# Kernel optimization log

Hardware: AMD Instinct MI355X
Metric: run time of the kernel (lower is better)

## Reference

```python
import jax, jax.numpy as jnp
import numpy as np

DT_SCALER = 1.0 / 24.0
ODE_STEPS = 4  # fixed-step RK4 stand-in for adaptive odeint(rtol=atol=1e-3)
B, T, D, H = 1024, 100, 32, 256
ODE_MID = 50  # hidden width of the ODE func MLP (hard-coded 50 in source)


def setup_inputs() -> dict:
    key = jax.random.key(0)
    ks = jax.random.split(key, 20)
    n = lambda k, s: jax.random.normal(k, s, dtype=jnp.float32)
    std = 0.1  # module inits weights N(0, 0.1), biases 0
    return {
        "dt": jax.random.uniform(ks[0], (B, T, 2), dtype=jnp.float32),
        "x": n(ks[1], (B, T, D)),
        # RNNCell params
        "W_ih": n(ks[2], (H, D)) * std,
        "b_ih": jnp.zeros((H,), jnp.float32),
        "W_hh": n(ks[3], (H, H)) * std,
        "b_hh": jnp.zeros((H,), jnp.float32),
        # ODE func: Linear(H,50) -> tanh -> Linear(50,H)
        "ode_w1": n(ks[4], (ODE_MID, H)) * std,
        "ode_b1": jnp.zeros((ODE_MID,), jnp.float32),
        "ode_w2": n(ks[5], (H, ODE_MID)) * std,
        "ode_b2": jnp.zeros((H,), jnp.float32),
        # mu head: l1 (H -> H//2), distribution_mu (H//2 -> 1)
        "l1_w": n(ks[6], (H // 2, H)) * std,
        "l1_b": jnp.zeros((H // 2,), jnp.float32),
        "mu_w": n(ks[7], (1, H // 2)) * std,
        "mu_b": jnp.zeros((1,), jnp.float32),
        # sigma head: Linear(H,H) -> tanh -> Linear(H,1) -> softplus
        "sig_w1": n(ks[8], (H, H)) * std,
        "sig_b1": jnp.zeros((H,), jnp.float32),
        "sig_w2": n(ks[9], (1, H)) * std,
        "sig_b2": jnp.zeros((1,), jnp.float32),
    }


def reference(dt, x, W_ih, b_ih, W_hh, b_hh, ode_w1, ode_b1, ode_w2, ode_b2,
              l1_w, l1_b, mu_w, mu_b, sig_w1, sig_b1, sig_w2, sig_b2):
    Bsz = x.shape[0]
    xs = jnp.swapaxes(x, 0, 1)                               # [T,B,D]
    dts = jnp.swapaxes(dt[:, :, 1] - dt[:, :, 0], 0, 1)[..., None]  # [T,B,1]
    h0 = jnp.zeros((Bsz, W_hh.shape[0]), x.dtype)
    hs = 1.0 / ODE_STEPS

    def ode_f(y, scale):
        # net(y) * (dt * DT_SCALER); RHS is time-independent
        return (jnp.tanh(y @ ode_w1.T + ode_b1) @ ode_w2.T + ode_b2) * scale

    def step(h, inp):
        x_i, dt_i = inp                                      # [B,D], [B,1]
        # h_t = h_t + RNNCell(x_i, h_t)
        h = h + jnp.tanh(x_i @ W_ih.T + b_ih + h @ W_hh.T + b_hh)
        scale = dt_i * DT_SCALER
        # integrate dh/dt = ode_f(h) from t=0 to t=1 (fixed-step RK4)
        def rk4(y, _):
            k1 = ode_f(y, scale)
            k2 = ode_f(y + 0.5 * hs * k1, scale)
            k3 = ode_f(y + 0.5 * hs * k2, scale)
            k4 = ode_f(y + hs * k3, scale)
            return y + (hs / 6.0) * (k1 + 2.0 * k2 + 2.0 * k3 + k4), None
        h, _ = jax.lax.scan(rk4, h, None, length=ODE_STEPS)
        # heads (eval mode: dropout is identity)
        mu = jax.nn.relu(h @ l1_w.T + l1_b) @ mu_w.T + mu_b              # [B,1]
        sig = jax.nn.softplus(jnp.tanh(h @ sig_w1.T + sig_b1) @ sig_w2.T + sig_b2)
        return h, (mu, sig)

    _, (mu_seq, sig_seq) = jax.lax.scan(step, h0, (xs, dts))
    mu_out = jnp.swapaxes(mu_seq, 0, 1)    # [B,T,1]
    sig_out = jnp.swapaxes(sig_seq, 0, 1)  # [B,T,1]
    return (mu_out, sig_out)
```

## Files before the change

### kernel.cpp

```cpp
#include <hip/hip_runtime.h>
#include <math.h>


#define NT 512

#define WS_WCAT 0
#define WS_L1P  73728
#define WS_SW1  106496
#define WS_TOT  172032

#define SM_PR  0
#define SM_H   8192
#define SM_YC  8704
#define SM_AC  9216
#define SM_MD  9728
#define SM_X4  9856
#define SM_BC  9920
#define SM_OB1 10176
#define SM_OB2 10240
#define SM_L1B 10496
#define SM_SB1 10624
#define SM_MUW 10880
#define SM_SW2 11008
#define SM_SCL 11264
#define SM_TOT 11272
#define SMEM_BYTES (SM_TOT * 4)

__device__ __forceinline__ float fma4(float acc, float4 y, float4 w) {
  acc = fmaf(y.x, w.x, acc);
  acc = fmaf(y.y, w.y, acc);
  acc = fmaf(y.z, w.z, acc);
  acc = fmaf(y.w, w.w, acc);
  return acc;
}

__device__ __forceinline__ float4 add4(float4 a, float4 b) {
  return make_float4(a.x + b.x, a.y + b.y, a.z + b.z, a.w + b.w);
}

__device__ __forceinline__ float tfast(float x) {
  float ax = fabsf(x);
  float e  = __expf(-2.f * ax);
  float t  = (1.f - e) * __builtin_amdgcn_rcpf(1.f + e);
  return copysignf(t, x);
}

__device__ __forceinline__ float4 tfast4(float4 v) {
  return make_float4(tfast(v.x), tfast(v.y), tfast(v.z), tfast(v.w));
}

__global__ void prep_transpose(const float* __restrict__ Wih,
                               const float* __restrict__ Whh,
                               const float* __restrict__ l1w,
                               const float* __restrict__ sw1,
                               float* __restrict__ ws) {
  int i = blockIdx.x * 256 + threadIdx.x;
  if (i < 73728) {
    int g = i >> 10, rem = i & 1023, j = rem >> 2, c = rem & 3;
    int k = 4 * g + c;
    ws[i] = (k < 32) ? Wih[j * 32 + k] : Whh[j * 256 + (k - 32)];
  } else if (i < 106496) {
    int t = i - 73728;
    int g = t >> 9, rem = t & 511, j = rem >> 2, c = rem & 3;
    ws[i] = l1w[j * 256 + 4 * g + c];
  } else if (i < WS_TOT) {
    int t = i - 106496;
    int g = t >> 10, rem = t & 1023, j = rem >> 2, c = rem & 3;
    ws[i] = sw1[j * 256 + 4 * g + c];
  }
}

__global__ __attribute__((amdgpu_flat_work_group_size(NT, NT)))
__attribute__((amdgpu_waves_per_eu(4)))
void odernn_main(const float* __restrict__ dt,
                 const float* __restrict__ x,
                 const float* __restrict__ bih,
                 const float* __restrict__ bhh,
                 const float* __restrict__ ow1,
                 const float* __restrict__ ob1g,
                 const float* __restrict__ ow2,
                 const float* __restrict__ ob2g,
                 const float* __restrict__ l1bg,
                 const float* __restrict__ muwg,
                 const float* __restrict__ mubg,
                 const float* __restrict__ sb1g,
                 const float* __restrict__ sw2g,
                 const float* __restrict__ sb2g,
                 const float* __restrict__ ws,
                 float* __restrict__ out) {
  extern __shared__ __align__(16) float sm[];
  const int tid = threadIdx.x;
  const int wv = tid >> 6, ln = tid & 63;
  const int b0 = blockIdx.x * 2;

  float* hS   = sm + SM_H;
  float* x4S  = sm + SM_X4;
  float* bcS  = sm + SM_BC;
  float* ob1S = sm + SM_OB1;
  float* ob2S = sm + SM_OB2;
  float* l1bS = sm + SM_L1B;
  float* sb1S = sm + SM_SB1;
  float* muwS = sm + SM_MUW;
  float* sw2S = sm + SM_SW2;
  float* sclS = sm + SM_SCL;

  float4* pr4  = (float4*)(sm + SM_PR);
  float4* h4   = (float4*)(sm + SM_H);
  float4* yc4  = (float4*)(sm + SM_YC);
  float4* ac4  = (float4*)(sm + SM_AC);
  float4* md4w = (float4*)(sm + SM_MD);
  float4* l1o4 = (float4*)(sm + SM_YC);
  float4* sg4  = (float4*)(sm + SM_AC);
  const float4* h44  = (const float4*)(sm + SM_H);
  const float4* yc44 = (const float4*)(sm + SM_YC);
  const float4* md4  = (const float4*)(sm + SM_MD);
  const float4* x44  = (const float4*)(sm + SM_X4);
  const float4* bc4  = (const float4*)bcS;
  const float4* ob1_4 = (const float4*)ob1S;
  const float4* ob2_4 = (const float4*)ob2S;
  const float4* l1b4 = (const float4*)l1bS;
  const float4* sb14 = (const float4*)sb1S;
  const float4* muw4 = (const float4*)muwS;
  const float4* sw24 = (const float4*)sw2S;

  const float4* wcat4 = (const float4*)(ws + WS_WCAT);
  const float4* l1w4  = (const float4*)(ws + WS_L1P);
  const float4* sw14  = (const float4*)(ws + WS_SW1);

  const int q1 = tid & 15, kc1 = tid >> 4;
  const int cq2 = tid & 63, kc2 = tid >> 6;
  float4 w1r[4][2];
  float4 w2r[4][2];
  {
#pragma unroll
    for (int n = 0; n < 4; ++n) {
      int row = 4 * q1 + n;
#pragma unroll
      for (int g = 0; g < 2; ++g) {
        if (row < 50)
          w1r[n][g] = *(const float4*)&ow1[row * 256 + kc1 * 8 + 4 * g];
        else
          w1r[n][g] = make_float4(0.f, 0.f, 0.f, 0.f);
      }
    }
    float w2tmp[4];
#pragma unroll
    for (int n = 0; n < 4; ++n) {
      int col = 4 * cq2 + n;
#pragma unroll
      for (int g = 0; g < 2; ++g) {
#pragma unroll
        for (int c = 0; c < 4; ++c) {
          int k = kc2 * 8 + 4 * g + c;
          w2tmp[c] = (k < 50) ? ow2[col * 50 + k] : 0.f;
        }
        w2r[n][g] = make_float4(w2tmp[0], w2tmp[1], w2tmp[2], w2tmp[3]);
      }
    }
  }

  if (tid < 256) {
    bcS[tid]  = bih[tid] + bhh[tid];
    ob2S[tid] = ob2g[tid];
    sb1S[tid] = sb1g[tid];
    sw2S[tid] = sw2g[tid];
  }
  if (tid < 64)  ob1S[tid] = (tid < 50) ? ob1g[tid] : 0.f;
  if (tid < 128) { l1bS[tid] = l1bg[tid]; muwS[tid] = muwg[tid]; }
  if (tid < 512) hS[tid] = 0.f;
  __syncthreads();

  const float mub = mubg[0], sb2 = sb2g[0];

  for (int t = 0; t < 100; ++t) {
    if (tid < 64) {
      int r = tid >> 5, kk = tid & 31;
      x4S[r * 32 + kk] = x[((size_t)(b0 + r) * 100 + t) * 32 + kk];
    }
    if (tid < 2) {
      const float* dp = dt + ((size_t)(b0 + tid) * 100 + t) * 2;
      sclS[tid] = (dp[1] - dp[0]) * (1.f / 24.f);
    }
    __syncthreads();

    {
      const int jq = tid & 63, kc = tid >> 6;
      float4 acc0 = make_float4(0, 0, 0, 0), acc1 = acc0;
#pragma unroll 3
      for (int gg = 0; gg < 9; ++gg) {
        int g = kc * 9 + gg;
        float4 w0 = wcat4[g * 256 + 4 * jq + 0];
        float4 w1 = wcat4[g * 256 + 4 * jq + 1];
        float4 w2 = wcat4[g * 256 + 4 * jq + 2];
        float4 w3 = wcat4[g * 256 + 4 * jq + 3];
        float4 y0 = (g < 8) ? x44[g]     : h44[g - 8];
        float4 y1 = (g < 8) ? x44[8 + g] : h44[64 + (g - 8)];
        acc0.x = fma4(acc0.x, y0, w0); acc0.y = fma4(acc0.y, y0, w1);
        acc0.z = fma4(acc0.z, y0, w2); acc0.w = fma4(acc0.w, y0, w3);
        acc1.x = fma4(acc1.x, y1, w0); acc1.y = fma4(acc1.y, y1, w1);
        acc1.z = fma4(acc1.z, y1, w2); acc1.w = fma4(acc1.w, y1, w3);
      }
      pr4[(kc * 2 + 0) * 64 + jq] = acc0;
      pr4[(kc * 2 + 1) * 64 + jq] = acc1;
    }
    __syncthreads();
    if (tid < 128) {
      const int r = tid >> 6, jq = tid & 63;
      float4 v = pr4[r * 64 + jq];
#pragma unroll
      for (int kc = 1; kc < 8; ++kc) v = add4(v, pr4[(kc * 2 + r) * 64 + jq]);
      v = add4(v, bc4[jq]);
      int o4 = r * 64 + jq;
      h4[o4] = add4(h4[o4], tfast4(v));
    }
    __syncthreads();

#pragma unroll 1
    for (int os = 0; os < 4; ++os) {
#pragma unroll
      for (int s = 0; s < 4; ++s) {
        {
          const float4* ysrc = (s == 0) ? h44 : yc44;
          float4 a0 = make_float4(0, 0, 0, 0), a1 = a0;
#pragma unroll
          for (int g = 0; g < 2; ++g) {
            float4 y0 = ysrc[kc1 * 2 + g];
            float4 y1 = ysrc[64 + kc1 * 2 + g];
            a0.x = fma4(a0.x, y0, w1r[0][g]); a0.y = fma4(a0.y, y0, w1r[1][g]);
            a0.z = fma4(a0.z, y0, w1r[2][g]); a0.w = fma4(a0.w, y0, w1r[3][g]);
            a1.x = fma4(a1.x, y1, w1r[0][g]); a1.y = fma4(a1.y, y1, w1r[1][g]);
            a1.z = fma4(a1.z, y1, w1r[2][g]); a1.w = fma4(a1.w, y1, w1r[3][g]);
          }
          pr4[(kc1 * 2 + 0) * 16 + q1] = a0;
          pr4[(kc1 * 2 + 1) * 16 + q1] = a1;
        }
        __syncthreads();
        if (tid < 128) {
          const int r = tid >> 6, sub = (tid >> 4) & 3, qq = tid & 15;
          float4 v = pr4[(sub * 8 * 2 + r) * 16 + qq];
#pragma unroll
          for (int i = 1; i < 8; ++i)
            v = add4(v, pr4[((sub * 8 + i) * 2 + r) * 16 + qq]);
          v.x += __shfl_xor(v.x, 16); v.y += __shfl_xor(v.y, 16);
          v.z += __shfl_xor(v.z, 16); v.w += __shfl_xor(v.w, 16);
          v.x += __shfl_xor(v.x, 32); v.y += __shfl_xor(v.y, 32);
          v.z += __shfl_xor(v.z, 32); v.w += __shfl_xor(v.w, 32);
          if (sub == 0)
            md4w[r * 16 + qq] = tfast4(add4(v, ob1_4[qq]));
        }
        __syncthreads();
        {
          float4 b0v = make_float4(0, 0, 0, 0), b1v = b0v;
#pragma unroll
          for (int g = 0; g < 2; ++g) {
            float4 m0 = md4[kc2 * 2 + g];
            float4 m1 = md4[16 + kc2 * 2 + g];
            b0v.x = fma4(b0v.x, m0, w2r[0][g]); b0v.y = fma4(b0v.y, m0, w2r[1][g]);
            b0v.z = fma4(b0v.z, m0, w2r[2][g]); b0v.w = fma4(b0v.w, m0, w2r[3][g]);
            b1v.x = fma4(b1v.x, m1, w2r[0][g]); b1v.y = fma4(b1v.y, m1, w2r[1][g]);
            b1v.z = fma4(b1v.z, m1, w2r[2][g]); b1v.w = fma4(b1v.w, m1, w2r[3][g]);
          }
          pr4[(kc2 * 2 + 0) * 64 + cq2] = b0v;
          pr4[(kc2 * 2 + 1) * 64 + cq2] = b1v;
        }
        __syncthreads();
        if (tid < 128) {
          const int r = tid >> 6, cq = tid & 63;
          float4 v = pr4[r * 64 + cq];
#pragma unroll
          for (int kc = 1; kc < 8; ++kc) v = add4(v, pr4[(kc * 2 + r) * 64 + cq]);
          v = add4(v, ob2_4[cq]);
          float sc = sclS[r];
          float4 kv = make_float4(v.x * sc, v.y * sc, v.z * sc, v.w * sc);
          int o4 = r * 64 + cq;
          if (s == 0) {
            ac4[o4] = kv;
            float4 hv = h4[o4];
            yc4[o4] = make_float4(hv.x + 0.125f * kv.x, hv.y + 0.125f * kv.y,
                                  hv.z + 0.125f * kv.z, hv.w + 0.125f * kv.w);
          } else if (s == 1) {
            float4 a = ac4[o4];
            ac4[o4] = make_float4(a.x + 2.f * kv.x, a.y + 2.f * kv.y,
                                  a.z + 2.f * kv.z, a.w + 2.f * kv.w);
            float4 hv = h4[o4];
            yc4[o4] = make_float4(hv.x + 0.125f * kv.x, hv.y + 0.125f * kv.y,
                                  hv.z + 0.125f * kv.z, hv.w + 0.125f * kv.w);
          } else if (s == 2) {
            float4 a = ac4[o4];
            ac4[o4] = make_float4(a.x + 2.f * kv.x, a.y + 2.f * kv.y,
                                  a.z + 2.f * kv.z, a.w + 2.f * kv.w);
            float4 hv = h4[o4];
            yc4[o4] = make_float4(hv.x + 0.25f * kv.x, hv.y + 0.25f * kv.y,
                                  hv.z + 0.25f * kv.z, hv.w + 0.25f * kv.w);
          } else {
            float4 a = ac4[o4];
            float4 hv = h4[o4];
            const float c6 = 0.25f / 6.f;
            h4[o4] = make_float4(hv.x + c6 * (a.x + kv.x), hv.y + c6 * (a.y + kv.y),
                                 hv.z + c6 * (a.z + kv.z), hv.w + c6 * (a.w + kv.w));
          }
        }
        __syncthreads();
      }
    }

    {
      const int cq = tid & 31, kc = tid >> 5;
      float4 c0 = make_float4(0, 0, 0, 0), c1 = c0;
#pragma unroll 2
      for (int g = 0; g < 4; ++g) {
        int kg = kc * 4 + g;
        float4 w0 = l1w4[kg * 128 + 4 * cq + 0];
        float4 w1 = l1w4[kg * 128 + 4 * cq + 1];
        float4 w2 = l1w4[kg * 128 + 4 * cq + 2];
        float4 w3 = l1w4[kg * 128 + 4 * cq + 3];
        float4 y0 = h44[kg], y1 = h44[64 + kg];
        c0.x = fma4(c0.x, y0, w0); c0.y = fma4(c0.y, y0, w1);
        c0.z = fma4(c0.z, y0, w2); c0.w = fma4(c0.w, y0, w3);
        c1.x = fma4(c1.x, y1, w0); c1.y = fma4(c1.y, y1, w1);
        c1.z = fma4(c1.z, y1, w2); c1.w = fma4(c1.w, y1, w3);
      }
      pr4[(kc * 2 + 0) * 32 + cq] = c0;
      pr4[(kc * 2 + 1) * 32 + cq] = c1;
    }
    {
      float4 d0 = make_float4(0, 0, 0, 0), d1 = d0;
#pragma unroll 2
      for (int g = 0; g < 8; ++g) {
        int kg = kc2 * 8 + g;
        float4 w0 = sw14[kg * 256 + 4 * cq2 + 0];
        float4 w1 = sw14[kg * 256 + 4 * cq2 + 1];
        float4 w2 = sw14[kg * 256 + 4 * cq2 + 2];
        float4 w3 = sw14[kg * 256 + 4 * cq2 + 3];
        float4 y0 = h44[kg], y1 = h44[64 + kg];
        d0.x = fma4(d0.x, y0, w0); d0.y = fma4(d0.y, y0, w1);
        d0.z = fma4(d0.z, y0, w2); d0.w = fma4(d0.w, y0, w3);
        d1.x = fma4(d1.x, y1, w0); d1.y = fma4(d1.y, y1, w1);
        d1.z = fma4(d1.z, y1, w2); d1.w = fma4(d1.w, y1, w3);
      }
      pr4[1024 + (kc2 * 2 + 0) * 64 + cq2] = d0;
      pr4[1024 + (kc2 * 2 + 1) * 64 + cq2] = d1;
    }
    __syncthreads();
    if (tid < 128) {
      const int r = tid >> 6, sub = (tid >> 5) & 1, cq = tid & 31;
      float4 v = pr4[(sub * 8 * 2 + r) * 32 + cq];
#pragma unroll
      for (int i = 1; i < 8; ++i)
        v = add4(v, pr4[((sub * 8 + i) * 2 + r) * 32 + cq]);
      v.x += __shfl_xor(v.x, 32); v.y += __shfl_xor(v.y, 32);
      v.z += __shfl_xor(v.z, 32); v.w += __shfl_xor(v.w, 32);
      if (sub == 0) {
        float4 b = l1b4[cq];
        l1o4[r * 32 + cq] = make_float4(fmaxf(v.x + b.x, 0.f), fmaxf(v.y + b.y, 0.f),
                                        fmaxf(v.z + b.z, 0.f), fmaxf(v.w + b.w, 0.f));
      }
    } else if (tid < 256) {
      const int t2 = tid - 128;
      const int r = t2 >> 6, cq = t2 & 63;
      float4 v = pr4[1024 + r * 64 + cq];
#pragma unroll
      for (int kc = 1; kc < 8; ++kc)
        v = add4(v, pr4[1024 + (kc * 2 + r) * 64 + cq]);
      sg4[r * 64 + cq] = tfast4(add4(v, sb14[cq]));
    }
    __syncthreads();
    if (wv < 2) {
      const int r = wv, c = ln & 31;
      float4 l = l1o4[r * 32 + c], w = muw4[c];
      float pm = (ln < 32) ? (l.x * w.x + l.y * w.y + l.z * w.z + l.w * w.w) : 0.f;
#pragma unroll
      for (int off = 32; off > 0; off >>= 1) pm += __shfl_down(pm, off);
      if (ln == 0) out[(size_t)(b0 + r) * 100 + t] = pm + mub;
    } else if (wv < 4) {
      const int r = wv - 2;
      float4 s4 = sg4[r * 64 + ln], w = sw24[ln];
      float ps = s4.x * w.x + s4.y * w.y + s4.z * w.z + s4.w * w.w;
#pragma unroll
      for (int off = 32; off > 0; off >>= 1) ps += __shfl_down(ps, off);
      if (ln == 0) {
        float z = ps + sb2;
        float sp = fmaxf(z, 0.f) + log1pf(expf(-fabsf(z)));
        out[(size_t)102400 + (size_t)(b0 + r) * 100 + t] = sp;
      }
    }
  }
}

extern "C" void kernel_launch(void* const* d_in, const int* in_sizes, int n_in,
                              void* d_out, int out_size, void* d_ws, size_t ws_size,
                              hipStream_t stream) {
  const float* dt  = (const float*)d_in[0];
  const float* x   = (const float*)d_in[1];
  const float* Wih = (const float*)d_in[2];
  const float* bih = (const float*)d_in[3];
  const float* Whh = (const float*)d_in[4];
  const float* bhh = (const float*)d_in[5];
  const float* ow1 = (const float*)d_in[6];
  const float* ob1 = (const float*)d_in[7];
  const float* ow2 = (const float*)d_in[8];
  const float* ob2 = (const float*)d_in[9];
  const float* l1w = (const float*)d_in[10];
  const float* l1b = (const float*)d_in[11];
  const float* muw = (const float*)d_in[12];
  const float* mub = (const float*)d_in[13];
  const float* sw1 = (const float*)d_in[14];
  const float* sb1 = (const float*)d_in[15];
  const float* sw2 = (const float*)d_in[16];
  const float* sb2 = (const float*)d_in[17];
  float* ws  = (float*)d_ws;
  float* out = (float*)d_out;

  hipFuncSetAttribute((const void*)odernn_main,
                      hipFuncAttributeMaxDynamicSharedMemorySize, SMEM_BYTES);

  prep_transpose<<<WS_TOT / 256, 256, 0, stream>>>(Wih, Whh, l1w, sw1, ws);
  odernn_main<<<512, NT, SMEM_BYTES, stream>>>(dt, x, bih, bhh, ow1, ob1, ow2, ob2,
                                               l1b, muw, mub, sb1, sw2, sb2, ws, out);
}
```

Baseline: 3.755 ms.

## Split ODE MLP layers across half-block producer/consumer groups with DPP reductions

Rewrites the main kernel so the first 256 threads compute the ODE first layer and the mu head, while the other 256 compute the second layer, RK4 update and sigma head. Each half is synchronised through a single shared buffer. Cross-lane partial-sum reductions now use DPP adds instead of shared-memory partial buffers plus extra reduce passes. The RNN weights are re-laid out so each thread reads a contiguous float4 stream. H is double-buffered, and x/dt for the next step are prefetched, with the aim of cutting the shared-memory footprint and barrier count. The divergent split relies on matched __syncthreads counts between the two groups, which is fragile.

```diff
diff --git a/kernel.cpp b/kernel.cpp
--- a/kernel.cpp
+++ b/kernel.cpp
@@ -4,69 +4,124 @@
 
 #define NT 512
 
-#define WS_WCAT 0
-#define WS_L1P  73728
-#define WS_SW1  106496
-#define WS_TOT  172032
-
-#define SM_PR  0
-#define SM_H   8192
-#define SM_YC  8704
-#define SM_AC  9216
-#define SM_MD  9728
-#define SM_X4  9856
-#define SM_BC  9920
-#define SM_OB1 10176
-#define SM_OB2 10240
-#define SM_L1B 10496
-#define SM_SB1 10624
-#define SM_MUW 10880
-#define SM_SW2 11008
-#define SM_SCL 11264
-#define SM_TOT 11272
-#define SMEM_BYTES (SM_TOT * 4)
+#define WF_WCAT 0
+#define WF_L1   18432
+#define WF_SG   26624
+
+#define F4_YC   0
+#define F4_MID  128
+#define F4_HL   160
+#define F4_X    416
+#define F4_L1O  432
+#define F4_SG   496
+#define SM_L1B  2496
+#define SM_SB1  2624
+#define SM_MUW  2880
+#define SM_SW2  3008
+#define SM_SCL  3264
+#define SM_TOTF 3272
 
 __device__ __forceinline__ float fma4(float acc, float4 y, float4 w) {
-  acc = fmaf(y.x, w.x, acc);
-  acc = fmaf(y.y, w.y, acc);
-  acc = fmaf(y.z, w.z, acc);
-  acc = fmaf(y.w, w.w, acc);
+  acc = fmaf(y.x, w.x, acc); acc = fmaf(y.y, w.y, acc);
+  acc = fmaf(y.z, w.z, acc); acc = fmaf(y.w, w.w, acc);
   return acc;
 }
-
 __device__ __forceinline__ float4 add4(float4 a, float4 b) {
   return make_float4(a.x + b.x, a.y + b.y, a.z + b.z, a.w + b.w);
 }
-
+__device__ __forceinline__ float4 axpy4(float a, float4 xv, float4 yv) {
+  return make_float4(fmaf(a, xv.x, yv.x), fmaf(a, xv.y, yv.y),
+                     fmaf(a, xv.z, yv.z), fmaf(a, xv.w, yv.w));
+}
+__device__ __forceinline__ float4 muls4(float4 v, float s) {
+  return make_float4(v.x * s, v.y * s, v.z * s, v.w * s);
+}
 __device__ __forceinline__ float tfast(float x) {
   float ax = fabsf(x);
   float e  = __expf(-2.f * ax);
   float t  = (1.f - e) * __builtin_amdgcn_rcpf(1.f + e);
   return copysignf(t, x);
 }
-
 __device__ __forceinline__ float4 tfast4(float4 v) {
   return make_float4(tfast(v.x), tfast(v.y), tfast(v.z), tfast(v.w));
 }
 
-__global__ void prep_transpose(const float* __restrict__ Wih,
-                               const float* __restrict__ Whh,
-                               const float* __restrict__ l1w,
-                               const float* __restrict__ sw1,
-                               float* __restrict__ ws) {
+template <int CTRL>
+__device__ __forceinline__ float dpp_add(float v) {
+  int s = __builtin_amdgcn_update_dpp(0, __float_as_int(v), CTRL, 0xF, 0xF, true);
+  return v + __int_as_float(s);
+}
+__device__ __forceinline__ float red2(float v)  { return dpp_add<0xB1>(v); }
+__device__ __forceinline__ float red4(float v)  { return dpp_add<0x4E>(dpp_add<0xB1>(v)); }
+__device__ __forceinline__ float red8(float v)  {
+  return dpp_add<0xB1>(dpp_add<0x4E>(dpp_add<0x141>(v)));
+}
+__device__ __forceinline__ float red16(float v) {
+  return dpp_add<0xB1>(dpp_add<0x4E>(dpp_add<0x141>(dpp_add<0x140>(v))));
+}
+
+__global__ void prep_w(const float* __restrict__ Wih, const float* __restrict__ Whh,
+                       const float* __restrict__ l1w, const float* __restrict__ sw1,
+                       float* __restrict__ ws) {
   int i = blockIdx.x * 256 + threadIdx.x;
   if (i < 73728) {
-    int g = i >> 10, rem = i & 1023, j = rem >> 2, c = rem & 3;
-    int k = 4 * g + c;
-    ws[i] = (k < 32) ? Wih[j * 32 + k] : Whh[j * 256 + (k - 32)];
-  } else if (i < 106496) {
+    int fi = i >> 2, comp = i & 3;
+    int j = fi >> 9, tw = fi & 511;
+    int c = j / 9, gg = j - c * 9;
+    int cq = tw >> 3, kc = tw & 7;
+    int k = 36 * kc + 4 * gg + comp, col = 4 * cq + c;
+    ws[i] = (k < 32) ? Wih[col * 32 + k] : Whh[col * 256 + (k - 32)];
+  } else if (i < 73728 + 32768) {
     int t = i - 73728;
-    int g = t >> 9, rem = t & 511, j = rem >> 2, c = rem & 3;
-    ws[i] = l1w[j * 256 + 4 * g + c];
-  } else if (i < WS_TOT) {
+    int fi = t >> 2, comp = t & 3;
+    int j = fi >> 7, tt = fi & 127;
+    int c = j >> 4, jj = j & 15;
+    int cq = tt >> 2, kc = tt & 3;
+    int k = 4 * (4 * jj + kc) + comp, col = 4 * cq + c;
+    ws[73728 + t] = l1w[col * 256 + k];
+  } else if (i < 172032) {
     int t = i - 106496;
-    int g = t >> 10, rem = t & 1023, j = rem >> 2, c = rem & 3;
-    ws[i] = sw1[j * 256 + 4 * g + c];
+    int fi = t >> 2, comp = t & 3;
+    int j = fi >> 7, tt = fi & 127;
+    int c = j >> 5, jj = j & 31;
+    int cq = tt >> 1, kc = tt & 1;
+    int k = 4 * (2 * jj + kc) + comp, col = 4 * cq + c;
+    ws[106496 + t] = sw1[col * 256 + k];
+  }
+}
+
+__device__ __forceinline__ void rnn_phase(int tid, int pOld, const float4* __restrict__ wc4,
+                                          float4* smf4, float4 bcR) {
+  const int cq = tid >> 3, kc = tid & 7;
+  float a0 = 0, a1 = 0, a2 = 0, a3 = 0, a4 = 0, a5 = 0, a6 = 0, a7 = 0;
+#pragma unroll 1
+  for (int gg = 0; gg < 9; ++gg) {
+    int g = kc * 9 + gg;
+    int i0 = (g < 8) ? (F4_X + g) : (F4_HL + pOld * 128 + (g - 8));
+    int i1 = (g < 8) ? (F4_X + 8 + g) : (F4_HL + pOld * 128 + 64 + (g - 8));
+    float4 y0 = smf4[i0];
+    float4 y1 = smf4[i1];
+    float4 w0 = wc4[(0 * 9 + gg) * 512 + tid];
+    float4 w1 = wc4[(1 * 9 + gg) * 512 + tid];
+    float4 w2 = wc4[(2 * 9 + gg) * 512 + tid];
+    float4 w3 = wc4[(3 * 9 + gg) * 512 + tid];
+    a0 = fma4(a0, y0, w0); a1 = fma4(a1, y0, w1);
+    a2 = fma4(a2, y0, w2); a3 = fma4(a3, y0, w3);
+    a4 = fma4(a4, y1, w0); a5 = fma4(a5, y1, w1);
+    a6 = fma4(a6, y1, w2); a7 = fma4(a7, y1, w3);
+  }
+  a0 = red8(a0); a1 = red8(a1); a2 = red8(a2); a3 = red8(a3);
+  a4 = red8(a4); a5 = red8(a5); a6 = red8(a6); a7 = red8(a7);
+  if (kc == 0) {
+    float4 h0 = smf4[F4_HL + pOld * 128 + cq];
+    float4 h1 = smf4[F4_HL + pOld * 128 + 64 + cq];
+    float4 n0 = add4(h0, tfast4(add4(make_float4(a0, a1, a2, a3), bcR)));
+    float4 n1 = add4(h1, tfast4(add4(make_float4(a4, a5, a6, a7), bcR)));
+    int pN = pOld ^ 1;
+    smf4[F4_HL + pN * 128 + cq] = n0;
+    smf4[F4_HL + pN * 128 + 64 + cq] = n1;
+    smf4[F4_YC + cq] = n0;
+    smf4[F4_YC + 64 + cq] = n1;
   }
 }
 
@@ -88,300 +143,222 @@
                  const float* __restrict__ sb2g,
                  const float* __restrict__ ws,
                  float* __restrict__ out) {
-  extern __shared__ __align__(16) float sm[];
+  __shared__ __align__(16) float sm[SM_TOTF];
+  float4* smf4 = (float4*)sm;
   const int tid = threadIdx.x;
-  const int wv = tid >> 6, ln = tid & 63;
   const int b0 = blockIdx.x * 2;
 
-  float* hS   = sm + SM_H;
-  float* x4S  = sm + SM_X4;
-  float* bcS  = sm + SM_BC;
-  float* ob1S = sm + SM_OB1;
-  float* ob2S = sm + SM_OB2;
-  float* l1bS = sm + SM_L1B;
-  float* sb1S = sm + SM_SB1;
-  float* muwS = sm + SM_MUW;
-  float* sw2S = sm + SM_SW2;
-  float* sclS = sm + SM_SCL;
-
-  float4* pr4  = (float4*)(sm + SM_PR);
-  float4* h4   = (float4*)(sm + SM_H);
-  float4* yc4  = (float4*)(sm + SM_YC);
-  float4* ac4  = (float4*)(sm + SM_AC);
-  float4* md4w = (float4*)(sm + SM_MD);
-  float4* l1o4 = (float4*)(sm + SM_YC);
-  float4* sg4  = (float4*)(sm + SM_AC);
-  const float4* h44  = (const float4*)(sm + SM_H);
-  const float4* yc44 = (const float4*)(sm + SM_YC);
-  const float4* md4  = (const float4*)(sm + SM_MD);
-  const float4* x44  = (const float4*)(sm + SM_X4);
-  const float4* bc4  = (const float4*)bcS;
-  const float4* ob1_4 = (const float4*)ob1S;
-  const float4* ob2_4 = (const float4*)ob2S;
-  const float4* l1b4 = (const float4*)l1bS;
-  const float4* sb14 = (const float4*)sb1S;
-  const float4* muw4 = (const float4*)muwS;
-  const float4* sw24 = (const float4*)sw2S;
-
-  const float4* wcat4 = (const float4*)(ws + WS_WCAT);
-  const float4* l1w4  = (const float4*)(ws + WS_L1P);
-  const float4* sw14  = (const float4*)(ws + WS_SW1);
-
-  const int q1 = tid & 15, kc1 = tid >> 4;
-  const int cq2 = tid & 63, kc2 = tid >> 6;
-  float4 w1r[4][2];
-  float4 w2r[4][2];
-  {
+  const float4* wc4  = (const float4*)ws + WF_WCAT;
+  const float4* l1s4 = (const float4*)ws + WF_L1;
+  const float4* sgs4 = (const float4*)ws + WF_SG;
+
+  const int cqR = tid >> 3;
+  float4 bcR = make_float4(bih[4 * cqR + 0] + bhh[4 * cqR + 0],
+                           bih[4 * cqR + 1] + bhh[4 * cqR + 1],
+                           bih[4 * cqR + 2] + bhh[4 * cqR + 2],
+                           bih[4 * cqR + 3] + bhh[4 * cqR + 3]);
+
+  if (tid < 128) { sm[SM_L1B + tid] = l1bg[tid]; sm[SM_MUW + tid] = muwg[tid]; }
+  if (tid < 256) { sm[SM_SB1 + tid] = sb1g[tid]; sm[SM_SW2 + tid] = sw2g[tid]; }
+  if (tid < 128) smf4[F4_HL + tid] = make_float4(0.f, 0.f, 0.f, 0.f);
+  if (tid < 16) {
+    int r = tid >> 3, g = tid & 7;
+    smf4[F4_X + tid] = ((const float4*)x)[((size_t)(b0 + r) * 100) * 8 + g];
+  } else if (tid < 18) {
+    const float* dp = dt + ((size_t)(b0 + tid - 16) * 100) * 2;
+    sm[SM_SCL + tid - 16] = (dp[1] - dp[0]) * (1.f / 24.f);
+  }
+  __syncthreads();
+
+  if (tid < 256) {
+    const int q1 = tid >> 4, kc1 = tid & 15;
+    float4 w1r[16];
 #pragma unroll
     for (int n = 0; n < 4; ++n) {
       int row = 4 * q1 + n;
 #pragma unroll
-      for (int g = 0; g < 2; ++g) {
-        if (row < 50)
-          w1r[n][g] = *(const float4*)&ow1[row * 256 + kc1 * 8 + 4 * g];
-        else
-          w1r[n][g] = make_float4(0.f, 0.f, 0.f, 0.f);
-      }
+      for (int j = 0; j < 4; ++j)
+        w1r[n * 4 + j] = (row < 50)
+            ? *(const float4*)&ow1[row * 256 + 64 * j + 4 * kc1]
+            : make_float4(0.f, 0.f, 0.f, 0.f);
     }
-    float w2tmp[4];
-#pragma unroll
-    for (int n = 0; n < 4; ++n) {
-      int col = 4 * cq2 + n;
-#pragma unroll
-      for (int g = 0; g < 2; ++g) {
-#pragma unroll
-        for (int c = 0; c < 4; ++c) {
-          int k = kc2 * 8 + 4 * g + c;
-          w2tmp[c] = (k < 50) ? ow2[col * 50 + k] : 0.f;
-        }
-        w2r[n][g] = make_float4(w2tmp[0], w2tmp[1], w2tmp[2], w2tmp[3]);
+    float4 ob1r = make_float4(4 * q1 + 0 < 50 ? ob1g[4 * q1 + 0] : 0.f,
+                              4 * q1 + 1 < 50 ? ob1g[4 * q1 + 1] : 0.f,
+                              4 * q1 + 2 < 50 ? ob1g[4 * q1 + 2] : 0.f,
+                              4 * q1 + 3 < 50 ? ob1g[4 * q1 + 3] : 0.f);
+    const int rH = tid >> 7, cqH = (tid >> 2) & 31, kcH = tid & 3;
+    const int t7 = tid & 127;
+    const float mubv = mubg[0];
+
+    for (int t = 0; t < 100; ++t) {
+      const int pOld = t & 1, pNew = pOld ^ 1;
+      rnn_phase(tid, pOld, wc4, smf4, bcR);
+      __syncthreads();
+#pragma unroll 1
+      for (int e = 0; e < 16; ++e) {
+        float a0 = 0, a1 = 0, a2 = 0, a3 = 0, a4 = 0, a5 = 0, a6 = 0, a7 = 0;
+#pragma unroll
+        for (int j = 0; j < 4; ++j) {
+          float4 y0 = smf4[F4_YC + 16 * j + kc1];
+          float4 y1 = smf4[F4_YC + 64 + 16 * j + kc1];
+          a0 = fma4(a0, y0, w1r[0 * 4 + j]); a1 = fma4(a1, y0, w1r[1 * 4 + j]);
+          a2 = fma4(a2, y0, w1r[2 * 4 + j]); a3 = fma4(a3, y0, w1r[3 * 4 + j]);
+          a4 = fma4(a4, y1, w1r[0 * 4 + j]); a5 = fma4(a5, y1, w1r[1 * 4 + j]);
+          a6 = fma4(a6, y1, w1r[2 * 4 + j]); a7 = fma4(a7, y1, w1r[3 * 4 + j]);
+        }
+        a0 = red16(a0); a1 = red16(a1); a2 = red16(a2); a3 = red16(a3);
+        a4 = red16(a4); a5 = red16(a5); a6 = red16(a6); a7 = red16(a7);
+        if (kc1 == 0) {
+          smf4[F4_MID + q1]      = tfast4(add4(make_float4(a0, a1, a2, a3), ob1r));
+          smf4[F4_MID + 16 + q1] = tfast4(add4(make_float4(a4, a5, a6, a7), ob1r));
+        }
+        __syncthreads();
+        __syncthreads();
+      }
+      float c0 = 0, c1 = 0, c2 = 0, c3 = 0;
+#pragma unroll 2
+      for (int jj = 0; jj < 16; ++jj) {
+        float4 h = smf4[F4_HL + pNew * 128 + rH * 64 + 4 * jj + kcH];
+        c0 = fma4(c0, h, l1s4[(0 * 16 + jj) * 128 + t7]);
+        c1 = fma4(c1, h, l1s4[(1 * 16 + jj) * 128 + t7]);
+        c2 = fma4(c2, h, l1s4[(2 * 16 + jj) * 128 + t7]);
+        c3 = fma4(c3, h, l1s4[(3 * 16 + jj) * 128 + t7]);
+      }
+      c0 = red4(c0); c1 = red4(c1); c2 = red4(c2); c3 = red4(c3);
+      if (kcH == 0) {
+        float4 b = ((const float4*)(sm + SM_L1B))[cqH];
+        float4 v = add4(make_float4(c0, c1, c2, c3), b);
+        smf4[F4_L1O + rH * 32 + cqH] =
+            make_float4(fmaxf(v.x, 0.f), fmaxf(v.y, 0.f), fmaxf(v.z, 0.f), fmaxf(v.w, 0.f));
+      }
+      if (t < 99) {
+        if (tid < 16) {
+          int r = tid >> 3, g = tid & 7;
+          smf4[F4_X + tid] = ((const float4*)x)[((size_t)(b0 + r) * 100 + t + 1) * 8 + g];
+        } else if (tid < 18) {
+          const float* dp = dt + ((size_t)(b0 + tid - 16) * 100 + t + 1) * 2;
+          sm[SM_SCL + tid - 16] = (dp[1] - dp[0]) * (1.f / 24.f);
+        }
+      }
+      __syncthreads();
+      int wv = tid >> 6, ln = tid & 63;
+      if (wv < 2) {
+        float pm = 0.f;
+        if (ln < 32) {
+          float4 l = smf4[F4_L1O + wv * 32 + ln];
+          float4 w = ((const float4*)(sm + SM_MUW))[ln];
+          pm = l.x * w.x + l.y * w.y + l.z * w.z + l.w * w.w;
+        }
+#pragma unroll
+        for (int off = 32; off > 0; off >>= 1) pm += __shfl_down(pm, off);
+        if (ln == 0) out[(size_t)(b0 + wv) * 100 + t] = pm + mubv;
       }
     }
-  }
-
-  if (tid < 256) {
-    bcS[tid]  = bih[tid] + bhh[tid];
-    ob2S[tid] = ob2g[tid];
-    sb1S[tid] = sb1g[tid];
-    sw2S[tid] = sw2g[tid];
-  }
-  if (tid < 64)  ob1S[tid] = (tid < 50) ? ob1g[tid] : 0.f;
-  if (tid < 128) { l1bS[tid] = l1bg[tid]; muwS[tid] = muwg[tid]; }
-  if (tid < 512) hS[tid] = 0.f;
-  __syncthreads();
-
-  const float mub = mubg[0], sb2 = sb2g[0];
-
-  for (int t = 0; t < 100; ++t) {
-    if (tid < 64) {
-      int r = tid >> 5, kk = tid & 31;
-      x4S[r * 32 + kk] = x[((size_t)(b0 + r) * 100 + t) * 32 + kk];
+  } else {
+    const int tid2 = tid - 256;
+    const int cqB = tid2 >> 2, kc2 = tid2 & 3;
+    float4 w2r[16];
+#pragma unroll
+    for (int c = 0; c < 4; ++c) {
+      int col = 4 * cqB + c;
+#pragma unroll
+      for (int j = 0; j < 4; ++j) {
+        float w0v[4];
+#pragma unroll
+        for (int cc = 0; cc < 4; ++cc) {
+          int k = 16 * j + 4 * kc2 + cc;
+          w0v[cc] = (k < 50) ? ow2[col * 50 + k] : 0.f;
+        }
+        w2r[c * 4 + j] = make_float4(w0v[0], w0v[1], w0v[2], w0v[3]);
+      }
     }
-    if (tid < 2) {
-      const float* dp = dt + ((size_t)(b0 + tid) * 100 + t) * 2;
-      sclS[tid] = (dp[1] - dp[0]) * (1.f / 24.f);
-    }
-    __syncthreads();
-
-    {
-      const int jq = tid & 63, kc = tid >> 6;
-      float4 acc0 = make_float4(0, 0, 0, 0), acc1 = acc0;
-#pragma unroll 3
-      for (int gg = 0; gg < 9; ++gg) {
-        int g = kc * 9 + gg;
-        float4 w0 = wcat4[g * 256 + 4 * jq + 0];
-        float4 w1 = wcat4[g * 256 + 4 * jq + 1];
-        float4 w2 = wcat4[g * 256 + 4 * jq + 2];
-        float4 w3 = wcat4[g * 256 + 4 * jq + 3];
-        float4 y0 = (g < 8) ? x44[g]     : h44[g - 8];
-        float4 y1 = (g < 8) ? x44[8 + g] : h44[64 + (g - 8)];
-        acc0.x = fma4(acc0.x, y0, w0); acc0.y = fma4(acc0.y, y0, w1);
-        acc0.z = fma4(acc0.z, y0, w2); acc0.w = fma4(acc0.w, y0, w3);
-        acc1.x = fma4(acc1.x, y1, w0); acc1.y = fma4(acc1.y, y1, w1);
-        acc1.z = fma4(acc1.z, y1, w2); acc1.w = fma4(acc1.w, y1, w3);
-      }
-      pr4[(kc * 2 + 0) * 64 + jq] = acc0;
-      pr4[(kc * 2 + 1) * 64 + jq] = acc1;
-    }
-    __syncthreads();
-    if (tid < 128) {
-      const int r = tid >> 6, jq = tid & 63;
-      float4 v = pr4[r * 64 + jq];
-#pragma unroll
-      for (int kc = 1; kc < 8; ++kc) v = add4(v, pr4[(kc * 2 + r) * 64 + jq]);
-      v = add4(v, bc4[jq]);
-      int o4 = r * 64 + jq;
-      h4[o4] = add4(h4[o4], tfast4(v));
-    }
-    __syncthreads();
-
+    float4 ob2r = make_float4(ob2g[4 * cqB + 0], ob2g[4 * cqB + 1],
+                              ob2g[4 * cqB + 2], ob2g[4 * cqB + 3]);
+    const int rH = tid2 >> 7, cqH = (tid2 >> 1) & 63, kcH = tid2 & 1;
+    const int t7 = tid2 & 127;
+    const float sb2v = sb2g[0];
+
+    for (int t = 0; t < 100; ++t) {
+      const int pOld = t & 1, pNew = pOld ^ 1;
+      rnn_phase(tid, pOld, wc4, smf4, bcR);
+      __syncthreads();
+      float s0 = sm[SM_SCL + 0], s1 = sm[SM_SCL + 1];
+      float4 h0 = smf4[F4_YC + cqB];
+      float4 h1 = smf4[F4_YC + 64 + cqB];
+      float4 ac0 = make_float4(0, 0, 0, 0), ac1 = ac0;
 #pragma unroll 1
-    for (int os = 0; os < 4; ++os) {
-#pragma unroll
-      for (int s = 0; s < 4; ++s) {
-        {
-          const float4* ysrc = (s == 0) ? h44 : yc44;
-          float4 a0 = make_float4(0, 0, 0, 0), a1 = a0;
-#pragma unroll
-          for (int g = 0; g < 2; ++g) {
-            float4 y0 = ysrc[kc1 * 2 + g];
-            float4 y1 = ysrc[64 + kc1 * 2 + g];
-            a0.x = fma4(a0.x, y0, w1r[0][g]); a0.y = fma4(a0.y, y0, w1r[1][g]);
-            a0.z = fma4(a0.z, y0, w1r[2][g]); a0.w = fma4(a0.w, y0, w1r[3][g]);
-            a1.x = fma4(a1.x, y1, w1r[0][g]); a1.y = fma4(a1.y, y1, w1r[1][g]);
-            a1.z = fma4(a1.z, y1, w1r[2][g]); a1.w = fma4(a1.w, y1, w1r[3][g]);
+      for (int os = 0; os < 4; ++os) {
+#pragma unroll
+        for (int s = 0; s < 4; ++s) {
+          __syncthreads();
+          float b0 = 0, b1 = 0, b2 = 0, b3 = 0, b4 = 0, b5 = 0, b6 = 0, b7 = 0;
+#pragma unroll
+          for (int j = 0; j < 4; ++j) {
+            float4 m0 = smf4[F4_MID + 4 * j + kc2];
+            float4 m1 = smf4[F4_MID + 16 + 4 * j + kc2];
+            b0 = fma4(b0, m0, w2r[0 * 4 + j]); b1 = fma4(b1, m0, w2r[1 * 4 + j]);
+            b2 = fma4(b2, m0, w2r[2 * 4 + j]); b3 = fma4(b3, m0, w2r[3 * 4 + j]);
+            b4 = fma4(b4, m1, w2r[0 * 4 + j]); b5 = fma4(b5, m1, w2r[1 * 4 + j]);
+            b6 = fma4(b6, m1, w2r[2 * 4 + j]); b7 = fma4(b7, m1, w2r[3 * 4 + j]);
           }
-          pr4[(kc1 * 2 + 0) * 16 + q1] = a0;
-          pr4[(kc1 * 2 + 1) * 16 + q1] = a1;
-        }
-        __syncthreads();
-        if (tid < 128) {
-          const int r = tid >> 6, sub = (tid >> 4) & 3, qq = tid & 15;
-          float4 v = pr4[(sub * 8 * 2 + r) * 16 + qq];
-#pragma unroll
-          for (int i = 1; i < 8; ++i)
-            v = add4(v, pr4[((sub * 8 + i) * 2 + r) * 16 + qq]);
-          v.x += __shfl_xor(v.x, 16); v.y += __shfl_xor(v.y, 16);
-          v.z += __shfl_xor(v.z, 16); v.w += __shfl_xor(v.w, 16);
-          v.x += __shfl_xor(v.x, 32); v.y += __shfl_xor(v.y, 32);
-          v.z += __shfl_xor(v.z, 32); v.w += __shfl_xor(v.w, 32);
-          if (sub == 0)
-            md4w[r * 16 + qq] = tfast4(add4(v, ob1_4[qq]));
-        }
-        __syncthreads();
-        {
-          float4 b0v = make_float4(0, 0, 0, 0), b1v = b0v;
-#pragma unroll
-          for (int g = 0; g < 2; ++g) {
-            float4 m0 = md4[kc2 * 2 + g];
-            float4 m1 = md4[16 + kc2 * 2 + g];
-            b0v.x = fma4(b0v.x, m0, w2r[0][g]); b0v.y = fma4(b0v.y, m0, w2r[1][g]);
-            b0v.z = fma4(b0v.z, m0, w2r[2][g]); b0v.w = fma4(b0v.w, m0, w2r[3][g]);
-            b1v.x = fma4(b1v.x, m1, w2r[0][g]); b1v.y = fma4(b1v.y, m1, w2r[1][g]);
-            b1v.z = fma4(b1v.z, m1, w2r[2][g]); b1v.w = fma4(b1v.w, m1, w2r[3][g]);
+          b0 = red4(b0); b1 = red4(b1); b2 = red4(b2); b3 = red4(b3);
+          b4 = red4(b4); b5 = red4(b5); b6 = red4(b6); b7 = red4(b7);
+          float4 k0 = muls4(add4(make_float4(b0, b1, b2, b3), ob2r), s0);
+          float4 k1 = muls4(add4(make_float4(b4, b5, b6, b7), ob2r), s1);
+          float4 y0w, y1w;
+          if (s == 0) {
+            ac0 = k0; ac1 = k1;
+            y0w = axpy4(0.125f, k0, h0); y1w = axpy4(0.125f, k1, h1);
+          } else if (s == 1) {
+            ac0 = axpy4(2.f, k0, ac0); ac1 = axpy4(2.f, k1, ac1);
+            y0w = axpy4(0.125f, k0, h0); y1w = axpy4(0.125f, k1, h1);
+          } else if (s == 2) {
+            ac0 = axpy4(2.f, k0, ac0); ac1 = axpy4(2.f, k1, ac1);
+            y0w = axpy4(0.25f, k0, h0); y1w = axpy4(0.25f, k1, h1);
+          } else {
+            h0 = axpy4(0.25f / 6.f, add4(ac0, k0), h0);
+            h1 = axpy4(0.25f / 6.f, add4(ac1, k1), h1);
+            y0w = h0; y1w = h1;
           }
-          pr4[(kc2 * 2 + 0) * 64 + cq2] = b0v;
-          pr4[(kc2 * 2 + 1) * 64 + cq2] = b1v;
-        }
-        __syncthreads();
-        if (tid < 128) {
-          const int r = tid >> 6, cq = tid & 63;
-          float4 v = pr4[r * 64 + cq];
-#pragma unroll
-          for (int kc = 1; kc < 8; ++kc) v = add4(v, pr4[(kc * 2 + r) * 64 + cq]);
-          v = add4(v, ob2_4[cq]);
-          float sc = sclS[r];
-          float4 kv = make_float4(v.x * sc, v.y * sc, v.z * sc, v.w * sc);
-          int o4 = r * 64 + cq;
-          if (s == 0) {
-            ac4[o4] = kv;
-            float4 hv = h4[o4];
-            yc4[o4] = make_float4(hv.x + 0.125f * kv.x, hv.y + 0.125f * kv.y,
-                                  hv.z + 0.125f * kv.z, hv.w + 0.125f * kv.w);
-          } else if (s == 1) {
-            float4 a = ac4[o4];
-            ac4[o4] = make_float4(a.x + 2.f * kv.x, a.y + 2.f * kv.y,
-                                  a.z + 2.f * kv.z, a.w + 2.f * kv.w);
-            float4 hv = h4[o4];
-            yc4[o4] = make_float4(hv.x + 0.125f * kv.x, hv.y + 0.125f * kv.y,
-                                  hv.z + 0.125f * kv.z, hv.w + 0.125f * kv.w);
-          } else if (s == 2) {
-            float4 a = ac4[o4];
-            ac4[o4] = make_float4(a.x + 2.f * kv.x, a.y + 2.f * kv.y,
-                                  a.z + 2.f * kv.z, a.w + 2.f * kv.w);
-            float4 hv = h4[o4];
-            yc4[o4] = make_float4(hv.x + 0.25f * kv.x, hv.y + 0.25f * kv.y,
-                                  hv.z + 0.25f * kv.z, hv.w + 0.25f * kv.w);
-          } else {
-            float4 a = ac4[o4];
-            float4 hv = h4[o4];
-            const float c6 = 0.25f / 6.f;
-            h4[o4] = make_float4(hv.x + c6 * (a.x + kv.x), hv.y + c6 * (a.y + kv.y),
-                                 hv.z + c6 * (a.z + kv.z), hv.w + c6 * (a.w + kv.w));
+          if (kc2 == 0) {
+            smf4[F4_YC + cqB] = y0w;
+            smf4[F4_YC + 64 + cqB] = y1w;
+            if (os == 3 && s == 3) {
+              smf4[F4_HL + pNew * 128 + cqB] = h0;
+              smf4[F4_HL + pNew * 128 + 64 + cqB] = h1;
+            }
           }
-        }
-        __syncthreads();
-      }
-    }
-
-    {
-      const int cq = tid & 31, kc = tid >> 5;
-      float4 c0 = make_float4(0, 0, 0, 0), c1 = c0;
+          __syncthreads();
+        }
+      }
+      float d0 = 0, d1 = 0, d2 = 0, d3 = 0;
 #pragma unroll 2
-      for (int g = 0; g < 4; ++g) {
-        int kg = kc * 4 + g;
-        float4 w0 = l1w4[kg * 128 + 4 * cq + 0];
-        float4 w1 = l1w4[kg * 128 + 4 * cq + 1];
-        float4 w2 = l1w4[kg * 128 + 4 * cq + 2];
-        float4 w3 = l1w4[kg * 128 + 4 * cq + 3];
-        float4 y0 = h44[kg], y1 = h44[64 + kg];
-        c0.x = fma4(c0.x, y0, w0); c0.y = fma4(c0.y, y0, w1);
-        c0.z = fma4(c0.z, y0, w2); c0.w = fma4(c0.w, y0, w3);
-        c1.x = fma4(c1.x, y1, w0); c1.y = fma4(c1.y, y1, w1);
-        c1.z = fma4(c1.z, y1, w2); c1.w = fma4(c1.w, y1, w3);
-      }
-      pr4[(kc * 2 + 0) * 32 + cq] = c0;
-      pr4[(kc * 2 + 1) * 32 + cq] = c1;
-    }
-    {
-      float4 d0 = make_float4(0, 0, 0, 0), d1 = d0;
-#pragma unroll 2
-      for (int g = 0; g < 8; ++g) {
-        int kg = kc2 * 8 + g;
-        float4 w0 = sw14[kg * 256 + 4 * cq2 + 0];
-        float4 w1 = sw14[kg * 256 + 4 * cq2 + 1];
-        float4 w2 = sw14[kg * 256 + 4 * cq2 + 2];
-        float4 w3 = sw14[kg * 256 + 4 * cq2 + 3];
-        float4 y0 = h44[kg], y1 = h44[64 + kg];
-        d0.x = fma4(d0.x, y0, w0); d0.y = fma4(d0.y, y0, w1);
-        d0.z = fma4(d0.z, y0, w2); d0.w = fma4(d0.w, y0, w3);
-        d1.x = fma4(d1.x, y1, w0); d1.y = fma4(d1.y, y1, w1);
-        d1.z = fma4(d1.z, y1, w2); d1.w = fma4(d1.w, y1, w3);
-      }
-      pr4[1024 + (kc2 * 2 + 0) * 64 + cq2] = d0;
-      pr4[1024 + (kc2 * 2 + 1) * 64 + cq2] = d1;
-    }
-    __syncthreads();
-    if (tid < 128) {
-      const int r = tid >> 6, sub = (tid >> 5) & 1, cq = tid & 31;
-      float4 v = pr4[(sub * 8 * 2 + r) * 32 + cq];
-#pragma unroll
-      for (int i = 1; i < 8; ++i)
-        v = add4(v, pr4[((sub * 8 + i) * 2 + r) * 32 + cq]);
-      v.x += __shfl_xor(v.x, 32); v.y += __shfl_xor(v.y, 32);
-      v.z += __shfl_xor(v.z, 32); v.w += __shfl_xor(v.w, 32);
-      if (sub == 0) {
-        float4 b = l1b4[cq];
-        l1o4[r * 32 + cq] = make_float4(fmaxf(v.x + b.x, 0.f), fmaxf(v.y + b.y, 0.f),
-                                        fmaxf(v.z + b.z, 0.f), fmaxf(v.w + b.w, 0.f));
-      }
-    } else if (tid < 256) {
-      const int t2 = tid - 128;
-      const int r = t2 >> 6, cq = t2 & 63;
-      float4 v = pr4[1024 + r * 64 + cq];
-#pragma unroll
-      for (int kc = 1; kc < 8; ++kc)
-        v = add4(v, pr4[1024 + (kc * 2 + r) * 64 + cq]);
-      sg4[r * 64 + cq] = tfast4(add4(v, sb14[cq]));
-    }
-    __syncthreads();
-    if (wv < 2) {
-      const int r = wv, c = ln & 31;
-      float4 l = l1o4[r * 32 + c], w = muw4[c];
-      float pm = (ln < 32) ? (l.x * w.x + l.y * w.y + l.z * w.z + l.w * w.w) : 0.f;
-#pragma unroll
-      for (int off = 32; off > 0; off >>= 1) pm += __shfl_down(pm, off);
-      if (ln == 0) out[(size_t)(b0 + r) * 100 + t] = pm + mub;
-    } else if (wv < 4) {
-      const int r = wv - 2;
-      float4 s4 = sg4[r * 64 + ln], w = sw24[ln];
-      float ps = s4.x * w.x + s4.y * w.y + s4.z * w.z + s4.w * w.w;
-#pragma unroll
-      for (int off = 32; off > 0; off >>= 1) ps += __shfl_down(ps, off);
-      if (ln == 0) {
-        float z = ps + sb2;
-        float sp = fmaxf(z, 0.f) + log1pf(expf(-fabsf(z)));
-        out[(size_t)102400 + (size_t)(b0 + r) * 100 + t] = sp;
+      for (int jj = 0; jj < 32; ++jj) {
+        float4 h = smf4[F4_HL + pNew * 128 + rH * 64 + 2 * jj + kcH];
+        d0 = fma4(d0, h, sgs4[(0 * 32 + jj) * 128 + t7]);
+        d1 = fma4(d1, h, sgs4[(1 * 32 + jj) * 128 + t7]);
+        d2 = fma4(d2, h, sgs4[(2 * 32 + jj) * 128 + t7]);
+        d3 = fma4(d3, h, sgs4[(3 * 32 + jj) * 128 + t7]);
+      }
+      d0 = red2(d0); d1 = red2(d1); d2 = red2(d2); d3 = red2(d3);
+      if (kcH == 0) {
+        float4 sb = ((const float4*)(sm + SM_SB1))[cqH];
+        smf4[F4_SG + rH * 64 + cqH] = tfast4(add4(make_float4(d0, d1, d2, d3), sb));
+      }
+      __syncthreads();
+      int wv = tid >> 6, ln = tid & 63;
+      if (wv < 6) {
+        int r = wv - 4;
+        float4 sv = smf4[F4_SG + r * 64 + ln];
+        float4 w = ((const float4*)(sm + SM_SW2))[ln];
+        float ps = sv.x * w.x + sv.y * w.y + sv.z * w.z + sv.w * w.w;
+#pragma unroll
+        for (int off = 32; off > 0; off >>= 1) ps += __shfl_down(ps, off);
+        if (ln == 0) {
+          float z = ps + sb2v;
+          float sp = fmaxf(z, 0.f) + log1pf(expf(-fabsf(z)));
+          out[(size_t)102400 + (size_t)(b0 + r) * 100 + t] = sp;
+        }
       }
     }
   }
@@ -411,10 +388,7 @@
   float* ws  = (float*)d_ws;
   float* out = (float*)d_out;
 
-  hipFuncSetAttribute((const void*)odernn_main,
-                      hipFuncAttributeMaxDynamicSharedMemorySize, SMEM_BYTES);
-
-  prep_transpose<<<WS_TOT / 256, 256, 0, stream>>>(Wih, Whh, l1w, sw1, ws);
-  odernn_main<<<512, NT, SMEM_BYTES, stream>>>(dt, x, bih, bhh, ow1, ob1, ow2, ob2,
-                                               l1b, muw, mub, sb1, sw2, sb2, ws, out);
-}
+  prep_w<<<672, 256, 0, stream>>>(Wih, Whh, l1w, sw1, ws);
+  odernn_main<<<512, NT, 0, stream>>>(dt, x, bih, bhh, ow1, ob1, ow2, ob2,
+                                      l1b, muw, mub, sb1, sw2, sb2, ws, out);
+}
```

After: 3.806 ms. No clear change (+1.3%).
